# Kernel tuning notes

Measured on AMD Instinct MI355X. Metric: run time of the kernel, lower is better.

Reference implementation:

```python
import jax, jax.numpy as jnp
import numpy as np

N = 50000
E = 800000
IN_C = 128
HID = 32
OUT_C = 16
NEG_SLOPE = 0.2


def setup_inputs() -> dict:
    key = jax.random.key(0)
    ks = jax.random.split(key, 16)
    x = jax.random.normal(ks[0], (N, IN_C), dtype=jnp.float32)
    edge_index = jax.random.randint(ks[1], (2, E), 0, N, dtype=jnp.int64)

    def glorot(k, shape):
        fan = shape[0] + shape[-1]
        return jax.random.uniform(k, shape, jnp.float32, -1.0, 1.0) * jnp.sqrt(6.0 / fan)

    # layer1: in=128 -> heads=4, ch=32, concat -> out 128
    W1 = glorot(ks[2], (IN_C, 4 * HID))
    a_src1 = glorot(ks[3], (4, HID))
    a_dst1 = glorot(ks[4], (4, HID))
    b1 = jnp.zeros((4 * HID,), jnp.float32)
    # layer2: in=128 -> heads=2, ch=32, concat -> out 64
    W2 = glorot(ks[5], (4 * HID, 2 * HID))
    a_src2 = glorot(ks[6], (2, HID))
    a_dst2 = glorot(ks[7], (2, HID))
    b2 = jnp.zeros((2 * HID,), jnp.float32)
    # layer3: in=64 -> heads=1, ch=16, mean -> out 16
    W3 = glorot(ks[8], (2 * HID, OUT_C))
    a_src3 = glorot(ks[9], (1, OUT_C))
    a_dst3 = glorot(ks[10], (1, OUT_C))
    b3 = jnp.zeros((OUT_C,), jnp.float32)
    return {"x": x, "edge_index": edge_index,
            "W1": W1, "a_src1": a_src1, "a_dst1": a_dst1, "b1": b1,
            "W2": W2, "a_src2": a_src2, "a_dst2": a_dst2, "b2": b2,
            "W3": W3, "a_src3": a_src3, "a_dst3": a_dst3, "b3": b3}


def gat_conv(x, src, dst, W, a_src, a_dst, bias, heads, ch, concat):
    n = x.shape[0]
    h = (x @ W).reshape(n, heads, ch)                      # [N,H,C]
    alpha_s = jnp.einsum('nhc,hc->nh', h, a_src)           # [N,H]
    alpha_d = jnp.einsum('nhc,hc->nh', h, a_dst)           # [N,H]
    logits = jax.nn.leaky_relu(alpha_s[src] + alpha_d[dst], NEG_SLOPE)  # [E,H]
    # segment softmax over edges sharing the same destination node
    m = jax.ops.segment_max(logits, dst, num_segments=n)
    m = jnp.where(jnp.isfinite(m), m, 0.0)
    e = jnp.exp(logits - m[dst])
    denom = jax.ops.segment_sum(e, dst, num_segments=n)
    alpha = e / (denom[dst] + 1e-16)                       # [E,H]
    msg = h[src] * alpha[:, :, None]                       # [E,H,C]
    out = jax.ops.segment_sum(msg, dst, num_segments=n)    # [N,H,C]
    out = out.reshape(n, heads * ch) if concat else out.mean(axis=1)
    return out + bias


def reference(x, edge_index, W1, a_src1, a_dst1, b1, W2, a_src2, a_dst2, b2, W3, a_src3, a_dst3, b3):
    n = x.shape[0]
    loops = jnp.arange(n, dtype=edge_index.dtype)
    src = jnp.concatenate([edge_index[0], loops])  # add self loops (PyG default)
    dst = jnp.concatenate([edge_index[1], loops])
    h = jax.nn.relu(gat_conv(x, src, dst, W1, a_src1, a_dst1, b1, 4, HID, True))
    h = jax.nn.relu(gat_conv(h, src, dst, W2, a_src2, a_dst2, b2, 2, HID, True))
    out = gat_conv(h, src, dst, W3, a_src3, a_dst3, b3, 1, OUT_C, False)
    return out
```

## Files before the change

### kernel.cpp

```cpp
#include <hip/hip_runtime.h>
#include <hip/hip_bf16.h>
#include <stdint.h>

#define NODES 50000
#define NEDGE 800000
#define TEDGE (NEDGE + NODES)
#define SBLK 25
#define GBLK ((NODES + 63) / 64)
#define CHNK 64
#define CSRCH 13312
#define HALFN 25088
#define NSTR (2 * HALFN)

typedef unsigned short u16;
typedef unsigned int u32;
typedef unsigned long long u64;
typedef short s16x8 __attribute__((ext_vector_type(8)));
typedef float f32x4 __attribute__((ext_vector_type(4)));

__device__ __forceinline__ float bf2f(u16 v) {
  return __uint_as_float(((u32)v) << 16);
}
__device__ __forceinline__ u16 f2bf(float f) {
  u32 u = __float_as_uint(f);
  u32 r = (u + 0x7FFFu + ((u >> 16) & 1u)) >> 16;
  return (u16)r;
}
__device__ __forceinline__ float lo16f(u32 w) { return __uint_as_float(w << 16); }
__device__ __forceinline__ float hi16f(u32 w) { return __uint_as_float(w & 0xFFFF0000u); }
__device__ __forceinline__ float lrelu(float x) {
  return (x > 0.f) ? x : 0.2f * x;
}
__device__ __forceinline__ int clampn(int v) {
  return ((u32)v < NODES) ? v : 0;
}
__device__ __forceinline__ float load1(const void* p, size_t i, bool fb) {
  return fb ? bf2f(((const u16*)p)[i]) : ((const float*)p)[i];
}
__device__ __forceinline__ u32 encf(float f) {
  u32 u = __float_as_uint(f);
  return (u & 0x80000000u) ? ~u : (u | 0x80000000u);
}
__device__ __forceinline__ float decf(u32 k) {
  u32 u = (k & 0x80000000u) ? (k & 0x7FFFFFFFu) : ~k;
  return __uint_as_float(u);
}

__global__ __launch_bounds__(256) void k_probe(
    const int* __restrict__ ei, const u16* __restrict__ xs16,
    int* __restrict__ flags,
    const void* __restrict__ W1, const void* __restrict__ W2,
    const void* __restrict__ W3, const void* __restrict__ as1,
    const void* __restrict__ ad1, const void* __restrict__ as2,
    const void* __restrict__ ad2, const void* __restrict__ as3,
    const void* __restrict__ ad3, u16* __restrict__ wt1,
    u16* __restrict__ wt2, u16* __restrict__ wt3, u16* __restrict__ wa1,
    u16* __restrict__ wa2, u16* __restrict__ wa3) {
  __shared__ int sfb;
  int t = threadIdx.x;
  int g = blockIdx.x * 256 + t;
  if (blockIdx.x == 0 && t >= 2 && t < 32) flags[t] = 0;
  if (t < 64) {
    int big = 0;
#pragma unroll
    for (int k = 0; k < 4; ++k) {
      u32 ex = (xs16[2 * (t * 4 + k)] >> 7) & 0xFF;
      big += (ex >= 0x90);
    }
#pragma unroll
    for (int off = 32; off >= 1; off >>= 1) big += __shfl_xor(big, off);
    if (t == 0) sfb = (big >= 8) ? 0 : 1;
    if (blockIdx.x == 0) {
      int odd = 0, even = 0;
#pragma unroll
      for (int k = 0; k < 4; ++k) {
        int idx = t + 64 * k;
        odd |= (ei[2 * idx + 1] != 0);
        even |= (ei[2 * idx] != 0);
      }
      u64 bo = __ballot(odd);
      u64 be = __ballot(even);
      if (t == 0) flags[0] = (bo == 0ull && be != 0ull) ? 1 : 0;
    }
  }
  __syncthreads();
  bool fb = sfb != 0;
  if (blockIdx.x == 0 && t == 0) flags[1] = fb ? 1 : 0;

  auto fidx = [](int n, int k, int KS) {
    int nt = n >> 4, lrow = n & 15, ks = k >> 5, quad = (k >> 3) & 3, j = k & 7;
    return ((size_t)((nt * KS + ks) * 64 + quad * 16 + lrow)) * 8 + j;
  };

  if (g < 16384) {
    int n = g >> 7, k = g & 127;
    wt1[fidx(n, k, 4)] = f2bf(load1(W1, (size_t)k * 128 + n, fb));
  } else if (g < 24576) {
    int r = g - 16384;
    int n = r >> 7, k = r & 127;
    wt2[fidx(n, k, 4)] = f2bf(load1(W2, (size_t)k * 64 + n, fb));
  } else if (g < 25600) {
    int r = g - 24576;
    int n = r >> 6, k = r & 63;
    wt3[fidx(n, k, 2)] = f2bf(load1(W3, (size_t)k * 16 + n, fb));
  } else if (g < 27648) {
    int e = g - 25600;
    int n = e >> 7, k = e & 127;
    float v = 0.f;
    if (n < 8) {
      int head = (n < 4) ? n : n - 4;
      const void* av = (n < 4) ? as1 : ad1;
      for (int c = 0; c < 32; ++c)
        v += load1(W1, (size_t)k * 128 + head * 32 + c, fb) *
             load1(av, head * 32 + c, fb);
    }
    wa1[fidx(n, k, 4)] = (n < 8) ? f2bf(v) : (u16)0;
  } else if (g < 29696) {
    int e = g - 27648;
    int n = e >> 7, k = e & 127;
    float v = 0.f;
    if (n < 4) {
      int head = (n < 2) ? n : n - 2;
      const void* av = (n < 2) ? as2 : ad2;
      for (int c = 0; c < 32; ++c)
        v += load1(W2, (size_t)k * 64 + head * 32 + c, fb) *
             load1(av, head * 32 + c, fb);
    }
    wa2[fidx(n, k, 4)] = (n < 4) ? f2bf(v) : (u16)0;
  } else if (g < 30720) {
    int e = g - 29696;
    int n = e >> 6, k = e & 63;
    float v = 0.f;
    if (n < 2) {
      const void* av = (n < 1) ? as3 : ad3;
      for (int c = 0; c < 16; ++c)
        v += load1(W3, (size_t)k * 16 + c, fb) * load1(av, c, fb);
    }
    wa3[fidx(n, k, 2)] = (n < 2) ? f2bf(v) : (u16)0;
  }
}

__global__ __launch_bounds__(1024) void k_hista(const int* __restrict__ ei,
                                                const int* __restrict__ flags,
                                                u32* __restrict__ sd,
                                                u16* __restrict__ rank16,
                                                u16* __restrict__ cnt) {
  __shared__ u32 hcnt[HALFN / 2];
  int b = blockIdx.x;
  int c = b >> 1, half = b & 1;
  int t = threadIdx.x;
  for (int i = t; i < HALFN / 2; i += 1024) hcnt[i] = 0;
  __syncthreads();
  bool odd = flags[0] != 0;
  int ebase = c * CSRCH;
  int nlo = half * HALFN;
#pragma unroll
  for (int i = 0; i < 13; ++i) {
    int e = ebase + i * 1024 + t;
    if (e < TEDGE) {
      int s, d;
      if (e < NEDGE) {
        if (odd) { s = ei[2 * e]; d = ei[2 * (NEDGE + e)]; }
        else { s = ei[e]; d = ei[NEDGE + e]; }
      } else {
        s = e - NEDGE; d = s;
      }
      s = clampn(s); d = clampn(d);
      if (half == 0) sd[e] = (u32)s | ((u32)d << 16);
      int li = d - nlo;
      if ((u32)li < HALFN) {
        u32 old = atomicAdd(&hcnt[li >> 1], 1u << (16 * (li & 1)));
        rank16[e] = (u16)((old >> (16 * (li & 1))) & 0xFFFFu);
      }
    }
  }
  __syncthreads();
  u32* crow = (u32*)(cnt + (size_t)c * NSTR + nlo);
  for (int i = t; i < HALFN / 2; i += 1024) crow[i] = hcnt[i];
}

__global__ __launch_bounds__(256) void k_fold(const u16* __restrict__ cnt,
                                              u16* __restrict__ basecnt,
                                              int* __restrict__ deg) {
  int n = blockIdx.x * 256 + threadIdx.x;
  if (n >= NODES) return;
  int acc = 0;
#pragma unroll 8
  for (int c = 0; c < CHNK; ++c) {
    u16 v = cnt[(size_t)c * NSTR + n];
    basecnt[(size_t)c * NSTR + n] = (u16)acc;
    acc += v;
  }
  deg[n] = acc;
}

__global__ __launch_bounds__(1024) void k_scan(const int* __restrict__ deg,
                                               int* __restrict__ rowptr,
                                               int* __restrict__ parts,
                                               int* __restrict__ counter) {
  __shared__ int swave[16];
  __shared__ int sbase, stot;
  int b = blockIdx.x, t = threadIdx.x;
  int lane = t & 63, w = t >> 6;
  int i0 = b * 2048 + t * 2;
  int v0 = (i0 < NODES) ? deg[i0] : 0;
  int v1 = (i0 + 1 < NODES) ? deg[i0 + 1] : 0;
  int local = v0 + v1;
  int x = local;
#pragma unroll
  for (int off = 1; off < 64; off <<= 1) {
    int y = __shfl_up(x, off);
    if (lane >= off) x += y;
  }
  if (lane == 63) swave[w] = x;
  __syncthreads();
  if (w == 0) {
    int wv = (lane < 16) ? swave[lane] : 0;
#pragma unroll
    for (int off = 1; off < 16; off <<= 1) {
      int y = __shfl_up(wv, off);
      if (lane >= off) wv += y;
    }
    if (lane == 15) {
      __hip_atomic_store(&parts[b], wv, __ATOMIC_RELAXED,
                         __HIP_MEMORY_SCOPE_AGENT);
      __hip_atomic_fetch_add(counter, 1, __ATOMIC_RELEASE,
                             __HIP_MEMORY_SCOPE_AGENT);
    }
    if (lane < 16) swave[lane] = wv;
  }
  __syncthreads();
  if (t == 0) {
    while (__hip_atomic_load(counter, __ATOMIC_ACQUIRE,
                             __HIP_MEMORY_SCOPE_AGENT) < SBLK)
      __builtin_amdgcn_s_sleep(2);
  }
  __syncthreads();
  if (w == 0) {
    int pv = (lane < SBLK) ? __hip_atomic_load(&parts[lane], __ATOMIC_RELAXED,
                                               __HIP_MEMORY_SCOPE_AGENT)
                           : 0;
    int pb = (lane < b) ? pv : 0;
#pragma unroll
    for (int off = 32; off >= 1; off >>= 1) {
      pb += __shfl_xor(pb, off);
      pv += __shfl_xor(pv, off);
    }
    if (lane == 0) { sbase = pb; stot = pv; }
  }
  __syncthreads();
  int run = sbase + ((w == 0) ? 0 : swave[w - 1]) + (x - local);
  if (i0 < NODES) rowptr[i0] = run;
  if (i0 + 1 < NODES) rowptr[i0 + 1] = run + v0;
  if (b == 0 && t == 0) rowptr[NODES] = stot;
}

__global__ __launch_bounds__(1024) void k_scatter(const u32* __restrict__ sd,
                                                  const u16* __restrict__ rank16,
                                                  const u16* __restrict__ basecnt,
                                                  const int* __restrict__ rowptr,
                                                  u16* __restrict__ srcs) {
  int c = blockIdx.x / 13;
  int r = blockIdx.x % 13;
  int e = c * CSRCH + r * 1024 + threadIdx.x;
  if (e >= TEDGE) return;
  u32 v = sd[e];
  int d = (int)(v >> 16);
  int pos = rowptr[d] + (int)basecnt[(size_t)c * NSTR + d] + (int)rank16[e];
  srcs[pos] = (u16)(v & 0xFFFFu);
}

template <int K, int N, int H, bool XEXT>
__global__ __launch_bounds__(256) void k_gmfma(const void* __restrict__ xin,
                                               const u16* __restrict__ wtf,
                                               const u16* __restrict__ waf,
                                               u16* __restrict__ hout,
                                               float* __restrict__ asg,
                                               float* __restrict__ adg,
                                               u32* __restrict__ gm,
                                               const int* __restrict__ flags,
                                               int M) {
  constexpr int KP = K + 8;
  constexpr int NT = N / 16;
  constexpr int KS = K / 32;
  constexpr int KG = K / 8;
  __shared__ u16 xlds[64 * KP];
  __shared__ u32 lmax[2 * H];
  int t = threadIdx.x;
  int row0 = blockIdx.x * 64;
  bool fb = flags[1] != 0;
  if (t < 2 * H) lmax[t] = 0;

  bool xbf = XEXT ? fb : true;
  for (int i = t; i < 64 * KG; i += 256) {
    int r = i / KG, kg = i % KG;
    int grow = row0 + r;
    if (grow >= M) grow = M - 1;
    if (xbf) {
      *(uint4*)&xlds[r * KP + kg * 8] =
          *(const uint4*)((const u16*)xin + (size_t)grow * K + kg * 8);
    } else {
      const float* gp = (const float*)xin + (size_t)grow * K + kg * 8;
      float4 f0 = *(const float4*)gp, f1 = *(const float4*)(gp + 4);
      *(ushort4*)&xlds[r * KP + kg * 8] =
          make_ushort4(f2bf(f0.x), f2bf(f0.y), f2bf(f0.z), f2bf(f0.w));
      *(ushort4*)&xlds[r * KP + kg * 8 + 4] =
          make_ushort4(f2bf(f1.x), f2bf(f1.y), f2bf(f1.z), f2bf(f1.w));
    }
  }
  __syncthreads();

  int lane = t & 63, w = t >> 6;
  int lrow = lane & 15, quad = lane >> 4;
  f32x4 acc[NT];
  f32x4 eacc = (f32x4){0.f, 0.f, 0.f, 0.f};
#pragma unroll
  for (int nt = 0; nt < NT; ++nt) acc[nt] = (f32x4){0.f, 0.f, 0.f, 0.f};

  const u16* xbase = xlds + (w * 16 + lrow) * KP + quad * 8;
#pragma unroll
  for (int ks = 0; ks < KS; ++ks) {
    s16x8 a = *(const s16x8*)(xbase + ks * 32);
    s16x8 be = *(const s16x8*)(waf + ((size_t)(ks * 64 + lane)) * 8);
    eacc = __builtin_amdgcn_mfma_f32_16x16x32_bf16(a, be, eacc, 0, 0, 0);
#pragma unroll
    for (int nt = 0; nt < NT; ++nt) {
      s16x8 b = *(const s16x8*)(wtf + ((size_t)((nt * KS + ks) * 64 + lane)) * 8);
      acc[nt] = __builtin_amdgcn_mfma_f32_16x16x32_bf16(a, b, acc[nt], 0, 0, 0);
    }
  }

  float pm = -3.4e38f;
  int baserow = row0 + w * 16 + quad * 4;
#pragma unroll
  for (int r = 0; r < 4; ++r) {
    int grow = baserow + r;
    if (grow < M) {
#pragma unroll
      for (int nt = 0; nt < NT; ++nt)
        hout[(size_t)grow * N + nt * 16 + lrow] = f2bf(acc[nt][r]);
      if (lrow < H) asg[grow * H + lrow] = eacc[r];
      else if (lrow < 2 * H) adg[grow * H + (lrow - H)] = eacc[r];
    }
    pm = fmaxf(pm, eacc[r]);
  }
  if (lrow < 2 * H) atomicMax(&lmax[lrow], encf(pm));
  __syncthreads();
  if (t < 2 * H) atomicMax(&gm[t], lmax[t]);
}

template <int H, int C, bool RELU, bool FINAL>
__global__ __launch_bounds__(256) void k_agg(const u16* __restrict__ hbuf,
                                             const float* __restrict__ asg,
                                             const float* __restrict__ adg,
                                             const int* __restrict__ rowptr,
                                             const u16* __restrict__ srcs,
                                             const void* __restrict__ bias,
                                             const int* __restrict__ flags,
                                             const u32* __restrict__ gm,
                                             void* __restrict__ outp, int n) {
  constexpr int HC = H * C;
  constexpr int L = HC / 8;
  constexpr int EPN = 32 / L;
  constexpr int UN = (4 * EPN <= 32) ? 4 : 2;
  __shared__ u16 lds_s[4][64];
  __shared__ float lds_e[4][64][H];
  int lane = threadIdx.x & 63;
  int w = threadIdx.x >> 6;
  int nh = lane >> 5;
  int hl = lane & 31;
  int node = blockIdx.x * 8 + w * 2 + nh;
  if (node >= n) node = n - 1;
  bool fb = flags[1] != 0;
  int start = rowptr[node], end = rowptr[node + 1];
  if (end < start || end - start > TEDGE) { start = 0; end = 0; }

  float adh[H], M[H];
#pragma unroll
  for (int h = 0; h < H; ++h) adh[h] = adg[node * H + h];
#pragma unroll
  for (int h = 0; h < H; ++h) M[h] = lrelu(decf(gm[h]) + decf(gm[H + h]));

  int sub = hl / L;
  int cl = hl & (L - 1);
  int ch0 = cl * 8;
  int myhead = ch0 / C;
  int base = nh * 32;

  float den[H];
#pragma unroll
  for (int h = 0; h < H; ++h) den[h] = 0.f;
  float acc[UN][8];
#pragma unroll
  for (int u = 0; u < UN; ++u)
#pragma unroll
    for (int i = 0; i < 8; ++i) acc[u][i] = 0.f;

  for (int chunk = start; chunk < end; chunk += 32) {
    int e = chunk + hl;
    int s = 0;
    float ee[H];
#pragma unroll
    for (int h = 0; h < H; ++h) ee[h] = 0.f;
    if (e < end) {
      s = srcs[e];
      float av[H];
      if (H == 4) { float4 t4 = *(const float4*)(asg + s * 4);
        av[0] = t4.x; av[1] = t4.y; av[H > 2 ? 2 : 0] = t4.z; av[H > 3 ? 3 : 0] = t4.w; }
      else if (H == 2) { float2 t2 = *(const float2*)(asg + s * 2); av[0] = t2.x; av[1] = t2.y; }
      else av[0] = asg[s];
#pragma unroll
      for (int h = 0; h < H; ++h) {
        float x = __expf(lrelu(av[h] + adh[h]) - M[h]);
        ee[h] = x;
        den[h] += x;
      }
    }
    __builtin_amdgcn_wave_barrier();
    lds_s[w][lane] = (u16)s;
#pragma unroll
    for (int h = 0; h < H; ++h) lds_e[w][lane][h] = ee[h];
    __builtin_amdgcn_wave_barrier();

    int cn = min(32, end - chunk);
    for (int j = 0; j < cn; j += UN * EPN) {
      int sx[UN];
      float ax[UN];
#pragma unroll
      for (int u = 0; u < UN; ++u) {
        int ei_ = base + j + u * EPN + sub;
        sx[u] = lds_s[w][ei_];
        ax[u] = lds_e[w][ei_][myhead];
      }
#pragma unroll
      for (int u = 0; u < UN; ++u) {
        uint4 v = *(const uint4*)(hbuf + (size_t)sx[u] * HC + ch0);
        acc[u][0] += ax[u] * lo16f(v.x); acc[u][1] += ax[u] * hi16f(v.x);
        acc[u][2] += ax[u] * lo16f(v.y); acc[u][3] += ax[u] * hi16f(v.y);
        acc[u][4] += ax[u] * lo16f(v.z); acc[u][5] += ax[u] * hi16f(v.z);
        acc[u][6] += ax[u] * lo16f(v.w); acc[u][7] += ax[u] * hi16f(v.w);
      }
    }
  }

#pragma unroll
  for (int m = 16; m >= 1; m >>= 1) {
#pragma unroll
    for (int h = 0; h < H; ++h) den[h] += __shfl_xor(den[h], m);
  }
  float tt[8];
#pragma unroll
  for (int i = 0; i < 8; ++i) {
    tt[i] = acc[0][i];
#pragma unroll
    for (int u = 1; u < UN; ++u) tt[i] += acc[u][i];
  }
#pragma unroll
  for (int m = L; m < 32; m <<= 1) {
#pragma unroll
    for (int i = 0; i < 8; ++i) tt[i] += __shfl_xor(tt[i], m);
  }

  if (sub == 0) {
    float inv = 1.f / (den[myhead] + 1e-16f);
    float o[8];
#pragma unroll
    for (int i = 0; i < 8; ++i) {
      o[i] = tt[i] * inv + load1(bias, ch0 + i, fb);
      if (RELU) o[i] = fmaxf(o[i], 0.f);
    }
    bool obf = FINAL ? fb : true;
    if (obf) {
      uint4 pk;
      pk.x = (u32)f2bf(o[0]) | ((u32)f2bf(o[1]) << 16);
      pk.y = (u32)f2bf(o[2]) | ((u32)f2bf(o[3]) << 16);
      pk.z = (u32)f2bf(o[4]) | ((u32)f2bf(o[5]) << 16);
      pk.w = (u32)f2bf(o[6]) | ((u32)f2bf(o[7]) << 16);
      *(uint4*)((u16*)outp + (size_t)node * HC + ch0) = pk;
    } else {
      float* op = (float*)outp + (size_t)node * HC + ch0;
      *(float4*)op = make_float4(o[0], o[1], o[2], o[3]);
      *(float4*)(op + 4) = make_float4(o[4], o[5], o[6], o[7]);
    }
  }
}


extern "C" void kernel_launch(void* const* d_in, const int* in_sizes, int n_in,
                              void* d_out, int out_size, void* d_ws, size_t ws_size,
                              hipStream_t stream) {
  const void* x   = d_in[0];
  const int* ei   = (const int*)d_in[1];
  const void* W1  = d_in[2];
  const void* as1 = d_in[3];
  const void* ad1 = d_in[4];
  const void* b1  = d_in[5];
  const void* W2  = d_in[6];
  const void* as2 = d_in[7];
  const void* ad2 = d_in[8];
  const void* b2  = d_in[9];
  const void* W3  = d_in[10];
  const void* as3 = d_in[11];
  const void* ad3 = d_in[12];
  const void* b3  = d_in[13];

  char* w = (char*)d_ws;
  auto alloc = [&](size_t bytes) {
    char* p = w;
    w += (bytes + 255) & ~(size_t)255;
    return p;
  };
  int* flags    = (int*)alloc(256);
  int* parts    = (int*)alloc(256);
  int* deg      = (int*)alloc((size_t)NODES * 4);
  int* rowptr   = (int*)alloc((size_t)(NODES + 1) * 4);
  u16* cnt      = (u16*)alloc((size_t)CHNK * NSTR * 2);
  u16* basecnt  = (u16*)alloc((size_t)CHNK * NSTR * 2);
  u32* sd       = (u32*)alloc((size_t)TEDGE * 4);
  u16* rank16   = (u16*)alloc((size_t)TEDGE * 2);
  u16* srcs     = (u16*)alloc((size_t)TEDGE * 2);
  float* asg    = (float*)alloc((size_t)NODES * 4 * 4);
  float* adg    = (float*)alloc((size_t)NODES * 4 * 4);
  u16* wt1      = (u16*)alloc((size_t)128 * 128 * 2);
  u16* wt2      = (u16*)alloc((size_t)64 * 128 * 2);
  u16* wt3      = (u16*)alloc((size_t)16 * 64 * 2);
  u16* wa1      = (u16*)alloc((size_t)16 * 128 * 2);
  u16* wa2      = (u16*)alloc((size_t)16 * 128 * 2);
  u16* wa3      = (u16*)alloc((size_t)16 * 64 * 2);
  u16* hbuf     = (u16*)alloc((size_t)NODES * 128 * 2);
  u16* obuf     = (u16*)alloc((size_t)NODES * 128 * 2);

  u32* gm1 = (u32*)(flags + 8);
  u32* gm2 = (u32*)(flags + 16);
  u32* gm3 = (u32*)(flags + 24);

  int ablocks = (NODES + 7) / 8;

  k_probe<<<(NODES + 255) / 256, 256, 0, stream>>>(
      ei, (const u16*)x, flags, W1, W2, W3, as1, ad1, as2, ad2, as3, ad3,
      wt1, wt2, wt3, wa1, wa2, wa3);
  k_hista<<<2 * CHNK, 1024, 0, stream>>>(ei, flags, sd, rank16, cnt);
  k_fold<<<(NODES + 255) / 256, 256, 0, stream>>>(cnt, basecnt, deg);
  k_scan<<<SBLK, 1024, 0, stream>>>(deg, rowptr, parts, flags + 2);
  k_scatter<<<CHNK * 13, 1024, 0, stream>>>(sd, rank16, basecnt, rowptr, srcs);

  k_gmfma<128, 128, 4, true><<<GBLK, 256, 0, stream>>>(x, wt1, wa1, hbuf, asg, adg, gm1, flags, NODES);
  k_agg<4, 32, true, false><<<ablocks, 256, 0, stream>>>(hbuf, asg, adg, rowptr, srcs, b1, flags, gm1, obuf, NODES);
  k_gmfma<128, 64, 2, false><<<GBLK, 256, 0, stream>>>(obuf, wt2, wa2, hbuf, asg, adg, gm2, flags, NODES);
  k_agg<2, 32, true, false><<<ablocks, 256, 0, stream>>>(hbuf, asg, adg, rowptr, srcs, b2, flags, gm2, obuf, NODES);
  k_gmfma<64, 16, 1, false><<<GBLK, 256, 0, stream>>>(obuf, wt3, wa3, hbuf, asg, adg, gm3, flags, NODES);
  k_agg<1, 16, false, true><<<ablocks, 256, 0, stream>>>(hbuf, asg, adg, rowptr, srcs, b3, flags, gm3, d_out, NODES);
}
```

Measured before the change: 265.4 us.

## Fuse fold with scan and co-schedule CSR scatter with layer-1 GEMM

Merges the per-node chunk-count fold into the decoupled scan kernel, with 64 blocks of 784 nodes each, so the deg array and one launch go away. The edge scatter is also merged with the first-layer MFMA projection in a single grid whose blocks alternate between scatter and GEMM roles, letting the memory-bound scatter overlap the compute-bound GEMM. This removes two launches and the idle gaps between them. The scan still relies on all 64 blocks being co-resident for its spin-wait, and the combined kernel now reserves GEMM-sized LDS for scatter blocks too.

```diff
diff --git a/kernel.cpp b/kernel.cpp
--- a/kernel.cpp
+++ b/kernel.cpp
@@ -5,12 +5,13 @@
 #define NODES 50000
 #define NEDGE 800000
 #define TEDGE (NEDGE + NODES)
-#define SBLK 25
 #define GBLK ((NODES + 63) / 64)
 #define CHNK 64
 #define CSRCH 13312
 #define HALFN 25088
 #define NSTR (2 * HALFN)
+#define FSB 64
+#define SCATB 832
 
 typedef unsigned short u16;
 typedef unsigned int u32;
@@ -179,34 +180,28 @@
   for (int i = t; i < HALFN / 2; i += 1024) crow[i] = hcnt[i];
 }
 
-__global__ __launch_bounds__(256) void k_fold(const u16* __restrict__ cnt,
-                                              u16* __restrict__ basecnt,
-                                              int* __restrict__ deg) {
-  int n = blockIdx.x * 256 + threadIdx.x;
-  if (n >= NODES) return;
-  int acc = 0;
-#pragma unroll 8
-  for (int c = 0; c < CHNK; ++c) {
-    u16 v = cnt[(size_t)c * NSTR + n];
-    basecnt[(size_t)c * NSTR + n] = (u16)acc;
-    acc += v;
-  }
-  deg[n] = acc;
-}
-
-__global__ __launch_bounds__(1024) void k_scan(const int* __restrict__ deg,
-                                               int* __restrict__ rowptr,
-                                               int* __restrict__ parts,
-                                               int* __restrict__ counter) {
+__global__ __launch_bounds__(1024) void k_foldscan(const u16* __restrict__ cnt,
+                                                   u16* __restrict__ basecnt,
+                                                   int* __restrict__ rowptr,
+                                                   int* __restrict__ parts,
+                                                   int* __restrict__ counter) {
   __shared__ int swave[16];
   __shared__ int sbase, stot;
   int b = blockIdx.x, t = threadIdx.x;
+  int n = b * 784 + t;
+  int v = 0;
+  if (t < 784 && n < NODES) {
+    int acc = 0;
+#pragma unroll 8
+    for (int c = 0; c < CHNK; ++c) {
+      u16 cv = cnt[(size_t)c * NSTR + n];
+      basecnt[(size_t)c * NSTR + n] = (u16)acc;
+      acc += cv;
+    }
+    v = acc;
+  }
   int lane = t & 63, w = t >> 6;
-  int i0 = b * 2048 + t * 2;
-  int v0 = (i0 < NODES) ? deg[i0] : 0;
-  int v1 = (i0 + 1 < NODES) ? deg[i0 + 1] : 0;
-  int local = v0 + v1;
-  int x = local;
+  int x = v;
 #pragma unroll
   for (int off = 1; off < 64; off <<= 1) {
     int y = __shfl_up(x, off);
@@ -232,14 +227,13 @@
   __syncthreads();
   if (t == 0) {
     while (__hip_atomic_load(counter, __ATOMIC_ACQUIRE,
-                             __HIP_MEMORY_SCOPE_AGENT) < SBLK)
+                             __HIP_MEMORY_SCOPE_AGENT) < FSB)
       __builtin_amdgcn_s_sleep(2);
   }
   __syncthreads();
   if (w == 0) {
-    int pv = (lane < SBLK) ? __hip_atomic_load(&parts[lane], __ATOMIC_RELAXED,
-                                               __HIP_MEMORY_SCOPE_AGENT)
-                           : 0;
+    int pv = __hip_atomic_load(&parts[lane], __ATOMIC_RELAXED,
+                               __HIP_MEMORY_SCOPE_AGENT);
     int pb = (lane < b) ? pv : 0;
 #pragma unroll
     for (int off = 32; off >= 1; off >>= 1) {
@@ -249,45 +243,29 @@
     if (lane == 0) { sbase = pb; stot = pv; }
   }
   __syncthreads();
-  int run = sbase + ((w == 0) ? 0 : swave[w - 1]) + (x - local);
-  if (i0 < NODES) rowptr[i0] = run;
-  if (i0 + 1 < NODES) rowptr[i0 + 1] = run + v0;
+  int run = sbase + ((w == 0) ? 0 : swave[w - 1]) + (x - v);
+  if (t < 784 && n < NODES) rowptr[n] = run;
   if (b == 0 && t == 0) rowptr[NODES] = stot;
 }
 
-__global__ __launch_bounds__(1024) void k_scatter(const u32* __restrict__ sd,
-                                                  const u16* __restrict__ rank16,
-                                                  const u16* __restrict__ basecnt,
-                                                  const int* __restrict__ rowptr,
-                                                  u16* __restrict__ srcs) {
-  int c = blockIdx.x / 13;
-  int r = blockIdx.x % 13;
-  int e = c * CSRCH + r * 1024 + threadIdx.x;
-  if (e >= TEDGE) return;
-  u32 v = sd[e];
-  int d = (int)(v >> 16);
-  int pos = rowptr[d] + (int)basecnt[(size_t)c * NSTR + d] + (int)rank16[e];
-  srcs[pos] = (u16)(v & 0xFFFFu);
-}
 
 template <int K, int N, int H, bool XEXT>
-__global__ __launch_bounds__(256) void k_gmfma(const void* __restrict__ xin,
-                                               const u16* __restrict__ wtf,
-                                               const u16* __restrict__ waf,
-                                               u16* __restrict__ hout,
-                                               float* __restrict__ asg,
-                                               float* __restrict__ adg,
-                                               u32* __restrict__ gm,
-                                               const int* __restrict__ flags,
-                                               int M) {
+__device__ __forceinline__ void gmfma_tile(const void* __restrict__ xin,
+                                           const u16* __restrict__ wtf,
+                                           const u16* __restrict__ waf,
+                                           u16* __restrict__ hout,
+                                           float* __restrict__ asg,
+                                           float* __restrict__ adg,
+                                           u32* __restrict__ gm,
+                                           const int* __restrict__ flags,
+                                           int M, int row0,
+                                           u16* __restrict__ xlds,
+                                           u32* __restrict__ lmax) {
   constexpr int KP = K + 8;
   constexpr int NT = N / 16;
   constexpr int KS = K / 32;
   constexpr int KG = K / 8;
-  __shared__ u16 xlds[64 * KP];
-  __shared__ u32 lmax[2 * H];
   int t = threadIdx.x;
-  int row0 = blockIdx.x * 64;
   bool fb = flags[1] != 0;
   if (t < 2 * H) lmax[t] = 0;
 
@@ -347,6 +325,55 @@
   if (lrow < 2 * H) atomicMax(&lmax[lrow], encf(pm));
   __syncthreads();
   if (t < 2 * H) atomicMax(&gm[t], lmax[t]);
+}
+
+__global__ __launch_bounds__(256) void k_scatgm(
+    const u32* __restrict__ sd, const u16* __restrict__ rank16,
+    const u16* __restrict__ basecnt, const int* __restrict__ rowptr,
+    u16* __restrict__ srcs, const void* __restrict__ xin,
+    const u16* __restrict__ wtf, const u16* __restrict__ waf,
+    u16* __restrict__ hout, float* __restrict__ asg, float* __restrict__ adg,
+    u32* __restrict__ gm, const int* __restrict__ flags) {
+  __shared__ u16 xlds[64 * 136];
+  __shared__ u32 lmax[8];
+  int bi = blockIdx.x;
+  int role, idx;
+  if (bi < 2 * GBLK) { role = bi & 1; idx = bi >> 1; }
+  else { role = 0; idx = GBLK + (bi - 2 * GBLK); }
+  if (role == 0) {
+    int c = idx / 13;
+    int e0 = idx * 1024 + threadIdx.x;
+#pragma unroll
+    for (int u = 0; u < 4; ++u) {
+      int e = e0 + u * 256;
+      if (e < TEDGE) {
+        u32 v = sd[e];
+        int d = (int)(v >> 16);
+        int pos = rowptr[d] + (int)basecnt[(size_t)c * NSTR + d] +
+                  (int)rank16[e];
+        srcs[pos] = (u16)(v & 0xFFFFu);
+      }
+    }
+    return;
+  }
+  gmfma_tile<128, 128, 4, true>(xin, wtf, waf, hout, asg, adg, gm, flags,
+                                NODES, idx * 64, xlds, lmax);
+}
+
+template <int K, int N, int H, bool XEXT>
+__global__ __launch_bounds__(256) void k_gmfma(const void* __restrict__ xin,
+                                               const u16* __restrict__ wtf,
+                                               const u16* __restrict__ waf,
+                                               u16* __restrict__ hout,
+                                               float* __restrict__ asg,
+                                               float* __restrict__ adg,
+                                               u32* __restrict__ gm,
+                                               const int* __restrict__ flags,
+                                               int M) {
+  __shared__ u16 xlds[64 * (K + 8)];
+  __shared__ u32 lmax[2 * H];
+  gmfma_tile<K, N, H, XEXT>(xin, wtf, waf, hout, asg, adg, gm, flags, M,
+                            blockIdx.x * 64, xlds, lmax);
 }
 
 template <int H, int C, bool RELU, bool FINAL>
@@ -512,7 +539,6 @@
   };
   int* flags    = (int*)alloc(256);
   int* parts    = (int*)alloc(256);
-  int* deg      = (int*)alloc((size_t)NODES * 4);
   int* rowptr   = (int*)alloc((size_t)(NODES + 1) * 4);
   u16* cnt      = (u16*)alloc((size_t)CHNK * NSTR * 2);
   u16* basecnt  = (u16*)alloc((size_t)CHNK * NSTR * 2);
@@ -535,16 +561,16 @@
   u32* gm3 = (u32*)(flags + 24);
 
   int ablocks = (NODES + 7) / 8;
+  int sgrid = 2 * GBLK + (SCATB - GBLK);
 
   k_probe<<<(NODES + 255) / 256, 256, 0, stream>>>(
       ei, (const u16*)x, flags, W1, W2, W3, as1, ad1, as2, ad2, as3, ad3,
       wt1, wt2, wt3, wa1, wa2, wa3);
   k_hista<<<2 * CHNK, 1024, 0, stream>>>(ei, flags, sd, rank16, cnt);
-  k_fold<<<(NODES + 255) / 256, 256, 0, stream>>>(cnt, basecnt, deg);
-  k_scan<<<SBLK, 1024, 0, stream>>>(deg, rowptr, parts, flags + 2);
-  k_scatter<<<CHNK * 13, 1024, 0, stream>>>(sd, rank16, basecnt, rowptr, srcs);
-
-  k_gmfma<128, 128, 4, true><<<GBLK, 256, 0, stream>>>(x, wt1, wa1, hbuf, asg, adg, gm1, flags, NODES);
+  k_foldscan<<<FSB, 1024, 0, stream>>>(cnt, basecnt, rowptr, parts, flags + 2);
+  k_scatgm<<<sgrid, 256, 0, stream>>>(sd, rank16, basecnt, rowptr, srcs,
+                                      x, wt1, wa1, hbuf, asg, adg, gm1, flags);
+
   k_agg<4, 32, true, false><<<ablocks, 256, 0, stream>>>(hbuf, asg, adg, rowptr, srcs, b1, flags, gm1, obuf, NODES);
   k_gmfma<128, 64, 2, false><<<GBLK, 256, 0, stream>>>(obuf, wt2, wa2, hbuf, asg, adg, gm2, flags, NODES);
   k_agg<2, 32, true, false><<<ablocks, 256, 0, stream>>>(hbuf, asg, adg, rowptr, srcs, b2, flags, gm2, obuf, NODES);
```

Result: faster. 255.3 us (-3.8%).
